# Kernel tuning notes

Hardware: AMD Instinct MI355X
Metric: run time of the kernel (lower is better)

Reference implementation:

```python
import jax, jax.numpy as jnp
import numpy as np

N_EMBD = 1024
N_HEAD = 16
HEAD_DIM = N_EMBD // N_HEAD  # 64
KV_RANK = 256
Q_RANK = 512
ROPE_DIM = 32
B, T = 2, 2048
EPS = 1e-6


def _rope_tables(T, dim):
    inv_freq = 1.0 / (10000.0 ** (np.arange(0, dim, 2, dtype=np.float32) / dim))
    t = np.arange(T, dtype=np.float32)
    freqs = np.outer(t, inv_freq)            # [T, dim/2]
    emb = np.concatenate([freqs, freqs], -1)  # [T, dim]
    return jnp.asarray(np.cos(emb)), jnp.asarray(np.sin(emb))


def _apply_rope(x, cos, sin):
    # x: [B, H, T, D]; cos/sin: [T, D]
    d2 = x.shape[-1] // 2
    x1, x2 = x[..., :d2], x[..., d2:]
    rot = jnp.concatenate([-x2, x1], axis=-1)
    return x * cos[None, None, :, :] + rot * sin[None, None, :, :]


def setup_inputs() -> dict:
    key = jax.random.key(0)
    ks = jax.random.split(key, 10)
    def w(k, fan_in, fan_out):
        return jax.random.normal(k, (fan_in, fan_out), dtype=jnp.float32) * (fan_in ** -0.5)
    return {
        "x": jax.random.normal(ks[0], (B, T, N_EMBD), dtype=jnp.float32),
        "W_kv": w(ks[1], N_EMBD, KV_RANK),
        "g_kv": jnp.ones((KV_RANK,), dtype=jnp.float32),
        "W_kdec": w(ks[2], KV_RANK, N_HEAD * HEAD_DIM),
        "W_vdec": w(ks[3], KV_RANK, N_HEAD * HEAD_DIM),
        "W_q": w(ks[4], N_EMBD, Q_RANK),
        "W_qdec": w(ks[5], Q_RANK, N_HEAD * HEAD_DIM),
        "W_krope": w(ks[6], N_EMBD, N_HEAD * ROPE_DIM),
        "W_qrope": w(ks[7], Q_RANK, N_HEAD * ROPE_DIM),
        "W_o": w(ks[8], N_HEAD * HEAD_DIM, N_EMBD),
    }


def reference(x, W_kv, g_kv, W_kdec, W_vdec, W_q, W_qdec, W_krope, W_qrope, W_o):
    Bx, Tx, C = x.shape
    # low-rank compression
    kv_c = x @ W_kv                                    # [B,T,R_kv]
    kv_c = kv_c * jax.lax.rsqrt(jnp.mean(kv_c * kv_c, axis=-1, keepdims=True) + EPS) * g_kv
    q_c = x @ W_q                                       # [B,T,R_q]
    # decompress to per-head content / rope parts -> [B,H,T,D]
    def heads(y, d):
        return y.reshape(Bx, Tx, N_HEAD, d).transpose(0, 2, 1, 3)
    k_content = heads(kv_c @ W_kdec, HEAD_DIM)
    v = heads(kv_c @ W_vdec, HEAD_DIM)
    q_content = heads(q_c @ W_qdec, HEAD_DIM)
    k_rope = heads(x @ W_krope, ROPE_DIM)
    q_rope = heads(q_c @ W_qrope, ROPE_DIM)
    cos, sin = _rope_tables(Tx, ROPE_DIM)
    q_rope = _apply_rope(q_rope, cos, sin)
    k_rope = _apply_rope(k_rope, cos, sin)
    q = jnp.concatenate([q_content, q_rope], axis=-1)   # [B,H,T,D+Dr]
    k = jnp.concatenate([k_content, k_rope], axis=-1)
    scale = 1.0 / jnp.sqrt(jnp.float32(q.shape[-1]))
    scores = jnp.einsum('bhqd,bhkd->bhqk', q, k) * scale  # [B,H,T,T]
    causal = jnp.tril(jnp.ones((Tx, Tx), dtype=bool))
    scores = jnp.where(causal[None, None], scores, jnp.float32(-jnp.inf))
    attn = jax.nn.softmax(scores, axis=-1)
    out = jnp.einsum('bhqk,bhkd->bhqd', attn, v)          # [B,H,T,D]
    out = out.transpose(0, 2, 1, 3).reshape(Bx, Tx, N_HEAD * HEAD_DIM)
    return out @ W_o
```

## Files before the change

### kernel.cpp

```cpp
#include <hip/hip_runtime.h>
#include <hip/hip_bf16.h>
#include <math.h>

#define Bz 2
#define Tz 2048
#define Cz 1024
#define Hz 16
#define Dz 64
#define Rz 32
#define KVR 256
#define QR 512
#define DQK 96
#define Mz (Bz*Tz)
#define BHT (Bz*Hz*Tz)
#define QK_SCALE 0.10206207261596577f
#define QK_SCALE2 0.14724538519399733f
#define THR2 11.541560327111707f

typedef __attribute__((ext_vector_type(8))) short short8;
typedef __attribute__((ext_vector_type(4))) float f32x4;
typedef __attribute__((ext_vector_type(4))) unsigned short ushort4v;

__device__ __forceinline__ unsigned short f2bf(float f) {
    union { float f; unsigned u; } un; un.f = f;
    unsigned r = un.u + 0x7FFF + ((un.u >> 16) & 1);
    return (unsigned short)(r >> 16);
}
__device__ __forceinline__ float bf2f(unsigned short h) {
    union { unsigned u; float f; } un; un.u = ((unsigned)h) << 16; return un.f;
}

__device__ __forceinline__ void gload_lds16(const void* g, void* l) {
    __builtin_amdgcn_global_load_lds(
        (const __attribute__((address_space(1))) unsigned int*)g,
        (__attribute__((address_space(3))) unsigned int*)l, 16, 0, 0);
}

__global__ __launch_bounds__(256) void conv_f32_bf16(const float* __restrict__ in,
                                                     unsigned short* __restrict__ out,
                                                     int n)
{
    int i = (blockIdx.x * 256 + threadIdx.x) * 4;
    if (i >= n) return;
    float4 v = *(const float4*)&in[i];
    ushort4v o = { f2bf(v.x), f2bf(v.y), f2bf(v.z), f2bf(v.w) };
    *(ushort4v*)&out[i] = o;
}

struct TDesc8 {
    const float* src[8];
    unsigned short* dst[8];
    int K[8], N[8];
    int tile0[9];
};

__global__ __launch_bounds__(256) void transpose_all(TDesc8 p)
{
    __shared__ float ts[32][33];
    int t = blockIdx.x;
    int wi = 0;
    #pragma unroll
    for (int i = 0; i < 7; i++) if (t >= p.tile0[i + 1]) wi = i + 1;
    int lt = t - p.tile0[wi];
    int K = p.K[wi], N = p.N[wi];
    int kT = K >> 5;
    int k0 = (lt % kT) * 32, n0 = (lt / kT) * 32;
    const float* in = p.src[wi];
    unsigned short* out = p.dst[wi];

    int tid = threadIdx.x;
    int r = tid >> 5, cc = tid & 31;
    #pragma unroll
    for (int l = 0; l < 4; l++)
        ts[r + l * 8][cc] = in[(size_t)(k0 + r + l * 8) * N + n0 + cc];
    __syncthreads();
    #pragma unroll
    for (int l = 0; l < 4; l++)
        out[(size_t)(n0 + r + l * 8) * K + k0 + cc] = f2bf(ts[cc][r + l * 8]);
}

template<int EMODE>
__global__ __launch_bounds__(64) void gemm1w(
    const unsigned short* __restrict__ A, const unsigned short* __restrict__ Wt,
    void* __restrict__ O0, void* __restrict__ O1, void* __restrict__ O2,
    int K, float scale)
{
    __shared__ __attribute__((aligned(16))) unsigned short As[64 * 64];
    __shared__ __attribute__((aligned(16))) unsigned short Bs[64 * 64];

    const int lane = threadIdx.x;
    const int c = lane & 15, g = lane >> 4;
    const int m0 = blockIdx.x * 64, n0 = blockIdx.y * 64;
    const int rl = lane >> 3, c8 = lane & 7;

    f32x4 acc[4][4] = {};

    auto stage = [&](int k0) {
        if (EMODE == 4) {
            int h = k0 >> 6;
            #pragma unroll
            for (int i = 0; i < 8; i++) {
                int m = m0 + i * 8 + rl;
                int b = m >> 11, t = m & (Tz - 1);
                gload_lds16(&A[(((size_t)b * Hz + h) * Tz + t) * 64 + c8 * 8],
                            &As[(i * 64 + lane) * 8]);
            }
        } else {
            #pragma unroll
            for (int i = 0; i < 8; i++)
                gload_lds16(&A[(size_t)(m0 + i * 8 + rl) * K + k0 + c8 * 8],
                            &As[(i * 64 + lane) * 8]);
        }
        #pragma unroll
        for (int i = 0; i < 8; i++)
            gload_lds16(&Wt[(size_t)(n0 + i * 8 + rl) * K + k0 + c8 * 8],
                        &Bs[(i * 64 + lane) * 8]);
    };

    stage(0);

    for (int k0 = 0; k0 < K; k0 += 64) {
        asm volatile("s_waitcnt vmcnt(0)" ::: "memory");
        __builtin_amdgcn_sched_barrier(0);

        short8 af[2][4], bfr[2][4];
        #pragma unroll
        for (int ks = 0; ks < 2; ks++) {
            #pragma unroll
            for (int mq = 0; mq < 4; mq++)
                af[ks][mq] = *(const short8*)&As[(mq * 16 + c) * 64 + ks * 32 + g * 8];
            #pragma unroll
            for (int nt = 0; nt < 4; nt++)
                bfr[ks][nt] = *(const short8*)&Bs[(nt * 16 + c) * 64 + ks * 32 + g * 8];
        }
        asm volatile("s_waitcnt lgkmcnt(0)" ::: "memory");
        __builtin_amdgcn_sched_barrier(0);

        if (k0 + 64 < K) stage(k0 + 64);

        __builtin_amdgcn_s_setprio(1);
        #pragma unroll
        for (int ks = 0; ks < 2; ks++)
            #pragma unroll
            for (int mq = 0; mq < 4; mq++)
                #pragma unroll
                for (int nt = 0; nt < 4; nt++)
                    acc[mq][nt] = __builtin_amdgcn_mfma_f32_16x16x32_bf16(
                        af[ks][mq], bfr[ks][nt], acc[mq][nt], 0, 0, 0);
        __builtin_amdgcn_s_setprio(0);
    }

    #pragma unroll
    for (int mq = 0; mq < 4; mq++) {
        #pragma unroll
        for (int r = 0; r < 4; r++) {
            int m = m0 + mq * 16 + g * 4 + r;
            int b = m >> 11, t = m & (Tz - 1);

            if (EMODE == 1) {
                if (n0 < 256) {
                    #pragma unroll
                    for (int nt = 0; nt < 4; nt++)
                        ((float*)O0)[(size_t)m * 256 + n0 + nt * 16 + c] = acc[mq][nt][r];
                } else if (n0 < 768) {
                    #pragma unroll
                    for (int nt = 0; nt < 4; nt++)
                        ((unsigned short*)O1)[(size_t)m * 512 + (n0 - 256) + nt * 16 + c] =
                            f2bf(acc[mq][nt][r]);
                } else {
                    float inv = __expf(-(float)c * 0.5756462732485114f);
                    float ang = (float)t * inv;
                    float cs = cosf(ang), sn = sinf(ang);
                    #pragma unroll
                    for (int np = 0; np < 4; np += 2) {
                        float v0 = acc[mq][np][r];
                        float v1 = acc[mq][np + 1][r];
                        int col0 = (n0 - 768) + np * 16;
                        int h = col0 >> 5;
                        size_t base = (((size_t)b * Hz + h) * Tz + t) * DQK + 64;
                        ((unsigned short*)O2)[base + c]      = f2bf(v0 * cs - v1 * sn);
                        ((unsigned short*)O2)[base + c + 16] = f2bf(v1 * cs + v0 * sn);
                    }
                }
            } else {
                #pragma unroll
                for (int nt = 0; nt < 4; nt++)
                    ((float*)O0)[(size_t)m * 1024 + n0 + nt * 16 + c] = acc[mq][nt][r];
            }
        }
    }
}

__global__ __launch_bounds__(64) void gemm1w23(
    const unsigned short* __restrict__ A2, const unsigned short* __restrict__ W2,
    unsigned short* __restrict__ qbb,
    const unsigned short* __restrict__ A3, const unsigned short* __restrict__ W3,
    unsigned short* __restrict__ kbb, unsigned short* __restrict__ vtb)
{
    const bool is2 = blockIdx.y < 24;
    const unsigned short* A  = is2 ? A2 : A3;
    const unsigned short* Wt = is2 ? W2 : W3;
    const int K = is2 ? QR : KVR;
    const int n0 = (is2 ? blockIdx.y : (blockIdx.y - 24)) * 64;

    __shared__ __attribute__((aligned(16))) unsigned short As[64 * 64];
    __shared__ __attribute__((aligned(16))) unsigned short Bs[64 * 64];

    const int lane = threadIdx.x;
    const int c = lane & 15, g = lane >> 4;
    const int m0 = blockIdx.x * 64;
    const int rl = lane >> 3, c8 = lane & 7;

    f32x4 acc[4][4] = {};

    auto stage = [&](int k0) {
        #pragma unroll
        for (int i = 0; i < 8; i++)
            gload_lds16(&A[(size_t)(m0 + i * 8 + rl) * K + k0 + c8 * 8],
                        &As[(i * 64 + lane) * 8]);
        #pragma unroll
        for (int i = 0; i < 8; i++)
            gload_lds16(&Wt[(size_t)(n0 + i * 8 + rl) * K + k0 + c8 * 8],
                        &Bs[(i * 64 + lane) * 8]);
    };

    stage(0);

    for (int k0 = 0; k0 < K; k0 += 64) {
        asm volatile("s_waitcnt vmcnt(0)" ::: "memory");
        __builtin_amdgcn_sched_barrier(0);

        short8 af[2][4], bfr[2][4];
        #pragma unroll
        for (int ks = 0; ks < 2; ks++) {
            #pragma unroll
            for (int mq = 0; mq < 4; mq++)
                af[ks][mq] = *(const short8*)&As[(mq * 16 + c) * 64 + ks * 32 + g * 8];
            #pragma unroll
            for (int nt = 0; nt < 4; nt++)
                bfr[ks][nt] = *(const short8*)&Bs[(nt * 16 + c) * 64 + ks * 32 + g * 8];
        }
        asm volatile("s_waitcnt lgkmcnt(0)" ::: "memory");
        __builtin_amdgcn_sched_barrier(0);

        if (k0 + 64 < K) stage(k0 + 64);

        __builtin_amdgcn_s_setprio(1);
        #pragma unroll
        for (int ks = 0; ks < 2; ks++)
            #pragma unroll
            for (int mq = 0; mq < 4; mq++)
                #pragma unroll
                for (int nt = 0; nt < 4; nt++)
                    acc[mq][nt] = __builtin_amdgcn_mfma_f32_16x16x32_bf16(
                        af[ks][mq], bfr[ks][nt], acc[mq][nt], 0, 0, 0);
        __builtin_amdgcn_s_setprio(0);
    }

    #pragma unroll
    for (int mq = 0; mq < 4; mq++) {
        #pragma unroll
        for (int r = 0; r < 4; r++) {
            int m = m0 + mq * 16 + g * 4 + r;
            int b = m >> 11, t = m & (Tz - 1);
            if (is2) {
                if (n0 < 1024) {
                    #pragma unroll
                    for (int nt = 0; nt < 4; nt++) {
                        int n = n0 + nt * 16 + c;
                        int h = n >> 6, dd = n & 63;
                        ((unsigned short*)qbb)[(((size_t)b * Hz + h) * Tz + t) * DQK + dd] =
                            f2bf(acc[mq][nt][r] * QK_SCALE2);
                    }
                } else {
                    float inv = __expf(-(float)c * 0.5756462732485114f);
                    float ang = (float)t * inv;
                    float cs = cosf(ang), sn = sinf(ang);
                    #pragma unroll
                    for (int np = 0; np < 4; np += 2) {
                        float v0 = acc[mq][np][r] * QK_SCALE2;
                        float v1 = acc[mq][np + 1][r] * QK_SCALE2;
                        int col0 = (n0 - 1024) + np * 16;
                        int h = col0 >> 5;
                        size_t base = (((size_t)b * Hz + h) * Tz + t) * DQK + 64;
                        qbb[base + c]      = f2bf(v0 * cs - v1 * sn);
                        qbb[base + c + 16] = f2bf(v1 * cs + v0 * sn);
                    }
                }
            } else {
                if (n0 < 1024) {
                    #pragma unroll
                    for (int nt = 0; nt < 4; nt++) {
                        int n = n0 + nt * 16 + c;
                        int h = n >> 6, dd = n & 63;
                        kbb[(((size_t)b * Hz + h) * Tz + t) * DQK + dd] = f2bf(acc[mq][nt][r]);
                    }
                } else {
                    #pragma unroll
                    for (int nt = 0; nt < 4; nt++) {
                        int n = (n0 - 1024) + nt * 16 + c;
                        int h = n >> 6, dd = n & 63;
                        vtb[(((size_t)b * Hz + h) * 64 + dd) * Tz + t] = f2bf(acc[mq][nt][r]);
                    }
                }
            }
        }
    }
}

__global__ __launch_bounds__(256) void rmsnorm_k(const float* __restrict__ kv,
                                                 const float* __restrict__ g,
                                                 unsigned short* __restrict__ outb)
{
    int row = blockIdx.x * 4 + (threadIdx.x >> 6);
    int lane = threadIdx.x & 63;
    const float* p = kv + (size_t)row * 256;
    float v[4];
    float ss = 0.f;
    #pragma unroll
    for (int i = 0; i < 4; i++) { v[i] = p[lane + i * 64]; ss += v[i] * v[i]; }
    #pragma unroll
    for (int o = 32; o > 0; o >>= 1) ss += __shfl_xor(ss, o);
    float r = rsqrtf(ss * (1.f / 256.f) + 1e-6f);
    #pragma unroll
    for (int i = 0; i < 4; i++)
        outb[(size_t)row * 256 + lane + i * 64] = f2bf(v[i] * r * g[lane + i * 64]);
}

#define PSTR 72

__global__ __launch_bounds__(256, 3) void attn_mfma(
    const unsigned short* __restrict__ q,
    const unsigned short* __restrict__ k,
    const unsigned short* __restrict__ vt,
    unsigned short* __restrict__ opart,
    float2* __restrict__ ml)
{
    __shared__ __attribute__((aligned(16))) unsigned short Ks[64 * 96];
    __shared__ __attribute__((aligned(16))) unsigned short Ps[4][16 * PSTR];

    int tid = threadIdx.x;
    int lane = tid & 63;
    int w = tid >> 6;
    int c = lane & 15, g = lane >> 4;

    int blk = blockIdx.x;
    int half = blk & 1;
    int s = blk >> 1;
    int bh = s & 31;
    int j = s >> 5;
    int qt = (j < 16) ? (31 - j) : (j - 16);
    int q0 = qt * 64;
    int ntiles = qt + 1;
    int nlo = ntiles >> 1;
    int tstart = half ? nlo : 0;
    int tend   = half ? ntiles : nlo;

    const unsigned short* qb = q + (size_t)bh * Tz * DQK;
    const unsigned short* kb = k + (size_t)bh * Tz * DQK;
    const unsigned short* vb = vt + (size_t)bh * 64 * Tz;
    unsigned short* ps = &Ps[w][0];

    int soff[3], sidx[3];
    #pragma unroll
    for (int i = 0; i < 3; i++) {
        int id2 = tid + i * 256;
        int srow = id2 / 12, sc8 = id2 % 12;
        soff[i] = srow * DQK + sc8 * 8;
        sidx[i] = (srow * 96 + sc8 * 8) ^ ((srow & 7) << 3);
    }

    short8 qf[3];
    {
        const unsigned short* qrow = qb + (size_t)(q0 + w * 16 + c) * DQK;
        #pragma unroll
        for (int kc = 0; kc < 3; kc++)
            qf[kc] = *(const short8*)(qrow + kc * 32 + g * 8);
    }

    short8 kreg[3];
    {
        size_t kix0 = (size_t)tstart * (64 * DQK);
        #pragma unroll
        for (int i = 0; i < 3; i++)
            kreg[i] = *(const short8*)&kb[kix0 + soff[i]];
        #pragma unroll
        for (int i = 0; i < 3; i++)
            *(short8*)&Ks[sidx[i]] = kreg[i];
    }
    __syncthreads();

    f32x4 oacc[4] = {};
    float mrun = -1e30f, lrun = 0.f;

    size_t kpre = (size_t)(tstart + 1) * (64 * DQK);
    size_t vix  = (size_t)c * Tz + g * 8 + (size_t)tstart * 64;

    for (int t = tstart; t < tend; t++) {
        bool more = (t + 1) < tend;

        if (more) {
            #pragma unroll
            for (int i = 0; i < 3; i++)
                kreg[i] = *(const short8*)&kb[kpre + soff[i]];
        }
        kpre += 64 * DQK;

        short8 vf[2][4];
        #pragma unroll
        for (int kc2 = 0; kc2 < 2; kc2++)
            #pragma unroll
            for (int nt = 0; nt < 4; nt++)
                vf[kc2][nt] = *(const short8*)&vb[vix + (size_t)nt * (16 * Tz) + kc2 * 32];
        vix += 64;

        f32x4 sacc[4] = {};
        __builtin_amdgcn_s_setprio(1);
        #pragma unroll
        for (int kc = 0; kc < 3; kc++) {
            #pragma unroll
            for (int nt = 0; nt < 4; nt++) {
                short8 kf = *(const short8*)&Ks[((nt * 16 + c) * 96 + kc * 32 + g * 8) ^ ((c & 7) << 3)];
                sacc[nt] = __builtin_amdgcn_mfma_f32_16x16x32_bf16(kf, qf[kc], sacc[nt], 0, 0, 0);
            }
        }
        __builtin_amdgcn_s_setprio(0);

        __syncthreads();
        if (more) {
            #pragma unroll
            for (int i = 0; i < 3; i++)
                *(short8*)&Ks[sidx[i]] = kreg[i];
        }

        if (t == ntiles - 1 && half) {
            #pragma unroll
            for (int nt = 0; nt < 4; nt++)
                #pragma unroll
                for (int r = 0; r < 4; r++)
                    if (nt * 16 + g * 4 + r > w * 16 + c)
                        sacc[nt][r] = -1e30f;
        }

        float pm = sacc[0][0];
        #pragma unroll
        for (int nt = 0; nt < 4; nt++)
            #pragma unroll
            for (int r = 0; r < 4; r++)
                pm = fmaxf(pm, sacc[nt][r]);
        pm = fmaxf(pm, __shfl_xor(pm, 16));
        pm = fmaxf(pm, __shfl_xor(pm, 32));

        bool need = pm > mrun + THR2;
        if (__ballot(need)) {
            float mn = fmaxf(mrun, pm);
            float sc = exp2f(mrun - mn);
            mrun = mn;
            float rs = 0.f;
            #pragma unroll
            for (int nt = 0; nt < 4; nt++)
                #pragma unroll
                for (int r = 0; r < 4; r++) {
                    sacc[nt][r] = exp2f(sacc[nt][r] - mrun);
                    rs += sacc[nt][r];
                }
            rs += __shfl_xor(rs, 16);
            rs += __shfl_xor(rs, 32);
            lrun = lrun * sc + rs;
            float scr[4];
            #pragma unroll
            for (int r = 0; r < 4; r++) scr[r] = __shfl(sc, g * 4 + r);
            #pragma unroll
            for (int nt = 0; nt < 4; nt++)
                #pragma unroll
                for (int r = 0; r < 4; r++)
                    oacc[nt][r] *= scr[r];
        } else {
            float rs = 0.f;
            #pragma unroll
            for (int nt = 0; nt < 4; nt++)
                #pragma unroll
                for (int r = 0; r < 4; r++) {
                    sacc[nt][r] = exp2f(sacc[nt][r] - mrun);
                    rs += sacc[nt][r];
                }
            rs += __shfl_xor(rs, 16);
            rs += __shfl_xor(rs, 32);
            lrun += rs;
        }

        #pragma unroll
        for (int nt = 0; nt < 4; nt++)
            #pragma unroll
            for (int rp = 0; rp < 2; rp++) {
                unsigned w32;
                asm("v_cvt_pk_bf16_f32 %0, %1, %2"
                    : "=v"(w32) : "v"(sacc[nt][2 * rp]), "v"(sacc[nt][2 * rp + 1]));
                *(unsigned*)&ps[c * PSTR + nt * 16 + g * 4 + 2 * rp] = w32;
            }
        __builtin_amdgcn_wave_barrier();

        __builtin_amdgcn_s_setprio(1);
        #pragma unroll
        for (int kc2 = 0; kc2 < 2; kc2++) {
            short8 pf = *(const short8*)&ps[c * PSTR + kc2 * 32 + g * 8];
            #pragma unroll
            for (int nt = 0; nt < 4; nt++)
                oacc[nt] = __builtin_amdgcn_mfma_f32_16x16x32_bf16(pf, vf[kc2][nt], oacc[nt], 0, 0, 0);
        }
        __builtin_amdgcn_s_setprio(0);
        __builtin_amdgcn_wave_barrier();

        __syncthreads();
    }

    size_t rowbase = (size_t)bh * Tz + q0 + w * 16;
    if (g == 0)
        ml[(size_t)half * BHT + rowbase + c] = make_float2(mrun, lrun);
    #pragma unroll
    for (int nt = 0; nt < 4; nt++)
        #pragma unroll
        for (int r = 0; r < 4; r++)
            opart[((size_t)half * BHT + rowbase + g * 4 + r) * 64 + nt * 16 + c] =
                f2bf(oacc[nt][r]);
}

__global__ __launch_bounds__(256) void attn_merge(
    const unsigned short* __restrict__ opart, const float2* __restrict__ ml,
    unsigned short* __restrict__ ob)
{
    size_t idx = (size_t)blockIdx.x * 256 + threadIdx.x;
    size_t row = idx >> 6;
    float2 a = ml[row], b = ml[BHT + row];
    float m = fmaxf(a.x, b.x);
    float s0 = exp2f(a.x - m), s1 = exp2f(b.x - m);
    float l = a.y * s0 + b.y * s1;
    float o0 = bf2f(opart[idx]), o1 = bf2f(opart[(size_t)BHT * 64 + idx]);
    ob[idx] = f2bf((o0 * s0 + o1 * s1) / l);
}

extern "C" void kernel_launch(void* const* d_in, const int* in_sizes, int n_in,
                              void* d_out, int out_size, void* d_ws, size_t ws_size,
                              hipStream_t stream)
{
    const float* x       = (const float*)d_in[0];
    const float* W_kv    = (const float*)d_in[1];
    const float* g_kv    = (const float*)d_in[2];
    const float* W_kdec  = (const float*)d_in[3];
    const float* W_vdec  = (const float*)d_in[4];
    const float* W_q     = (const float*)d_in[5];
    const float* W_qdec  = (const float*)d_in[6];
    const float* W_krope = (const float*)d_in[7];
    const float* W_qrope = (const float*)d_in[8];
    const float* W_o     = (const float*)d_in[9];
    float* out = (float*)d_out;

    float* kv_f32 = (float*)d_ws;
    unsigned short* us = (unsigned short*)(kv_f32 + (size_t)Mz * KVR);
    unsigned short* x_bf  = us;               us += (size_t)Mz * Cz;
    unsigned short* kv_bf = us;               us += (size_t)Mz * KVR;
    unsigned short* qc_bf = us;               us += (size_t)Mz * QR;
    unsigned short* qbb   = us;               us += (size_t)BHT * DQK;
    unsigned short* kbb   = us;               us += (size_t)BHT * DQK;
    unsigned short* vtb   = us;               us += (size_t)BHT * 64;
    unsigned short* ob    = us;               us += (size_t)BHT * 64;
    unsigned short* wc1 = us;                 us += (size_t)1280 * Cz;
    unsigned short* wc2 = us;                 us += (size_t)1536 * QR;
    unsigned short* wc3 = us;                 us += (size_t)2048 * KVR;
    unsigned short* woT = us;                 us += (size_t)Cz * Cz;
    unsigned short* opart = us;               us += (size_t)2 * BHT * 64;
    float2* mlbuf = (float2*)us;              us += (size_t)2 * BHT * 2;

    dim3 blk(256);

    conv_f32_bf16<<<dim3((Mz*Cz)/1024), blk, 0, stream>>>(x, x_bf, Mz*Cz);

    TDesc8 td;
    const float* tsrc[8] = {W_kv, W_q, W_krope, W_qdec, W_qrope, W_kdec, W_vdec, W_o};
    unsigned short* tdst[8] = {
        wc1, wc1 + (size_t)256 * Cz, wc1 + (size_t)768 * Cz,
        wc2, wc2 + (size_t)1024 * QR,
        wc3, wc3 + (size_t)1024 * KVR,
        woT };
    int tK[8] = {Cz, Cz, Cz, QR, QR, KVR, KVR, Cz};
    int tN[8] = {KVR, QR, Hz*Rz, Hz*Dz, Hz*Rz, Hz*Dz, Hz*Dz, Cz};
    int cum = 0;
    td.tile0[0] = 0;
    for (int i = 0; i < 8; i++) {
        td.src[i] = tsrc[i]; td.dst[i] = tdst[i]; td.K[i] = tK[i]; td.N[i] = tN[i];
        cum += (tK[i] / 32) * (tN[i] / 32);
        td.tile0[i + 1] = cum;
    }
    transpose_all<<<dim3(cum), blk, 0, stream>>>(td);

    gemm1w<1><<<dim3(Mz/64, 1280/64), dim3(64), 0, stream>>>(
        x_bf, wc1, kv_f32, qc_bf, kbb, Cz, 1.f);
    rmsnorm_k<<<dim3(Mz/4), blk, 0, stream>>>(kv_f32, g_kv, kv_bf);
    gemm1w23<<<dim3(Mz/64, 56), dim3(64), 0, stream>>>(
        qc_bf, wc2, qbb, kv_bf, wc3, kbb, vtb);
    attn_mfma<<<dim3(2048), blk, 0, stream>>>(qbb, kbb, vtb, opart, mlbuf);
    attn_merge<<<dim3((BHT * 64) / 256), blk, 0, stream>>>(opart, mlbuf, ob);
    gemm1w<4><<<dim3(Mz/64, Cz/64), dim3(64), 0, stream>>>(
        ob, woT, out, nullptr, nullptr, Cz, 1.f);
}
```

Before: 177.0 us.

## Drop split-KV attention and merge kernel; double-buffer K with overlapped QK and softmax

The attention kernel stops splitting each query tile's KV range across two blocks. It no longer writes partial outputs plus max/sum pairs for a separate merge kernel, and instead normalizes by the running sum and writes the final output directly. The K tile is double-buffered in LDS (KsA/KsB) so the QK MFMAs for the next tile are issued before softmax and PV of the current tile, overlapping matrix and vector work. This removes the merge launch and the partial-output traffic, but halves the grid to 1024 blocks and lowers the occupancy target to 2 blocks per CU, which may leave work unevenly spread across CUs.

```diff
diff --git a/kernel.cpp b/kernel.cpp
--- a/kernel.cpp
+++ b/kernel.cpp
@@ -329,14 +329,14 @@
 
 #define PSTR 72
 
-__global__ __launch_bounds__(256, 3) void attn_mfma(
+__global__ __launch_bounds__(256, 2) void attn_mfma(
     const unsigned short* __restrict__ q,
     const unsigned short* __restrict__ k,
     const unsigned short* __restrict__ vt,
-    unsigned short* __restrict__ opart,
-    float2* __restrict__ ml)
+    unsigned short* __restrict__ o)
 {
-    __shared__ __attribute__((aligned(16))) unsigned short Ks[64 * 96];
+    __shared__ __attribute__((aligned(16))) unsigned short KsA[64 * 96];
+    __shared__ __attribute__((aligned(16))) unsigned short KsB[64 * 96];
     __shared__ __attribute__((aligned(16))) unsigned short Ps[4][16 * PSTR];
 
     int tid = threadIdx.x;
@@ -344,17 +344,12 @@
     int w = tid >> 6;
     int c = lane & 15, g = lane >> 4;
 
-    int blk = blockIdx.x;
-    int half = blk & 1;
-    int s = blk >> 1;
+    int s = blockIdx.x;
     int bh = s & 31;
     int j = s >> 5;
     int qt = (j < 16) ? (31 - j) : (j - 16);
     int q0 = qt * 64;
     int ntiles = qt + 1;
-    int nlo = ntiles >> 1;
-    int tstart = half ? nlo : 0;
-    int tend   = half ? ntiles : nlo;
 
     const unsigned short* qb = q + (size_t)bh * Tz * DQK;
     const unsigned short* kb = k + (size_t)bh * Tz * DQK;
@@ -378,43 +373,11 @@
             qf[kc] = *(const short8*)(qrow + kc * 32 + g * 8);
     }
 
-    short8 kreg[3];
-    {
-        size_t kix0 = (size_t)tstart * (64 * DQK);
-        #pragma unroll
-        for (int i = 0; i < 3; i++)
-            kreg[i] = *(const short8*)&kb[kix0 + soff[i]];
-        #pragma unroll
-        for (int i = 0; i < 3; i++)
-            *(short8*)&Ks[sidx[i]] = kreg[i];
-    }
-    __syncthreads();
-
     f32x4 oacc[4] = {};
     float mrun = -1e30f, lrun = 0.f;
-
-    size_t kpre = (size_t)(tstart + 1) * (64 * DQK);
-    size_t vix  = (size_t)c * Tz + g * 8 + (size_t)tstart * 64;
-
-    for (int t = tstart; t < tend; t++) {
-        bool more = (t + 1) < tend;
-
-        if (more) {
-            #pragma unroll
-            for (int i = 0; i < 3; i++)
-                kreg[i] = *(const short8*)&kb[kpre + soff[i]];
-        }
-        kpre += 64 * DQK;
-
-        short8 vf[2][4];
-        #pragma unroll
-        for (int kc2 = 0; kc2 < 2; kc2++)
-            #pragma unroll
-            for (int nt = 0; nt < 4; nt++)
-                vf[kc2][nt] = *(const short8*)&vb[vix + (size_t)nt * (16 * Tz) + kc2 * 32];
-        vix += 64;
-
-        f32x4 sacc[4] = {};
+    f32x4 saccA[4] = {}, saccB[4] = {};
+
+    auto qk = [&](f32x4 (&sacc)[4], const unsigned short* Ks) {
         __builtin_amdgcn_s_setprio(1);
         #pragma unroll
         for (int kc = 0; kc < 3; kc++) {
@@ -425,15 +388,10 @@
             }
         }
         __builtin_amdgcn_s_setprio(0);
-
-        __syncthreads();
-        if (more) {
-            #pragma unroll
-            for (int i = 0; i < 3; i++)
-                *(short8*)&Ks[sidx[i]] = kreg[i];
-        }
-
-        if (t == ntiles - 1 && half) {
+    };
+
+    auto softmax_pv = [&](f32x4 (&sacc)[4], short8 (&vf)[2][4], bool diag) {
+        if (diag) {
             #pragma unroll
             for (int nt = 0; nt < 4; nt++)
                 #pragma unroll
@@ -441,7 +399,6 @@
                     if (nt * 16 + g * 4 + r > w * 16 + c)
                         sacc[nt][r] = -1e30f;
         }
-
         float pm = sacc[0][0];
         #pragma unroll
         for (int nt = 0; nt < 4; nt++)
@@ -510,33 +467,95 @@
         }
         __builtin_amdgcn_s_setprio(0);
         __builtin_amdgcn_wave_barrier();
-
+    };
+
+    short8 kreg[3];
+    #pragma unroll
+    for (int i = 0; i < 3; i++)
+        kreg[i] = *(const short8*)&kb[soff[i]];
+    #pragma unroll
+    for (int i = 0; i < 3; i++)
+        *(short8*)&KsA[sidx[i]] = kreg[i];
+    if (ntiles > 1) {
+        #pragma unroll
+        for (int i = 0; i < 3; i++)
+            kreg[i] = *(const short8*)&kb[(size_t)(64 * DQK) + soff[i]];
+    }
+    __syncthreads();
+    qk(saccA, KsA);
+
+    size_t kpre = (size_t)2 * (64 * DQK);
+    size_t vix  = (size_t)c * Tz + g * 8;
+
+    for (int t = 0; t < ntiles; t += 2) {
+        bool hasN1 = (t + 1) < ntiles;
+        bool hasN2 = (t + 2) < ntiles;
+        bool hasN3 = (t + 3) < ntiles;
+
+        if (hasN1) {
+            #pragma unroll
+            for (int i = 0; i < 3; i++)
+                *(short8*)&KsB[sidx[i]] = kreg[i];
+        }
+        if (hasN2) {
+            #pragma unroll
+            for (int i = 0; i < 3; i++)
+                kreg[i] = *(const short8*)&kb[kpre + soff[i]];
+        }
+        kpre += 64 * DQK;
         __syncthreads();
-    }
-
-    size_t rowbase = (size_t)bh * Tz + q0 + w * 16;
-    if (g == 0)
-        ml[(size_t)half * BHT + rowbase + c] = make_float2(mrun, lrun);
+
+        short8 vfA[2][4];
+        #pragma unroll
+        for (int kc2 = 0; kc2 < 2; kc2++)
+            #pragma unroll
+            for (int nt = 0; nt < 4; nt++)
+                vfA[kc2][nt] = *(const short8*)&vb[vix + (size_t)nt * (16 * Tz) + kc2 * 32];
+        vix += 64;
+
+        if (hasN1) qk(saccB, KsB);
+        softmax_pv(saccA, vfA, t == qt);
+        #pragma unroll
+        for (int nt = 0; nt < 4; nt++) saccA[nt] = f32x4{0.f, 0.f, 0.f, 0.f};
+
+        if (hasN1) {
+            if (hasN2) {
+                #pragma unroll
+                for (int i = 0; i < 3; i++)
+                    *(short8*)&KsA[sidx[i]] = kreg[i];
+            }
+            if (hasN3) {
+                #pragma unroll
+                for (int i = 0; i < 3; i++)
+                    kreg[i] = *(const short8*)&kb[kpre + soff[i]];
+            }
+            kpre += 64 * DQK;
+            __syncthreads();
+
+            short8 vfB[2][4];
+            #pragma unroll
+            for (int kc2 = 0; kc2 < 2; kc2++)
+                #pragma unroll
+                for (int nt = 0; nt < 4; nt++)
+                    vfB[kc2][nt] = *(const short8*)&vb[vix + (size_t)nt * (16 * Tz) + kc2 * 32];
+            vix += 64;
+
+            if (hasN2) qk(saccA, KsA);
+            softmax_pv(saccB, vfB, (t + 1) == qt);
+            #pragma unroll
+            for (int nt = 0; nt < 4; nt++) saccB[nt] = f32x4{0.f, 0.f, 0.f, 0.f};
+        }
+    }
+
+    float lr[4];
+    #pragma unroll
+    for (int r = 0; r < 4; r++) lr[r] = __shfl(lrun, g * 4 + r);
     #pragma unroll
     for (int nt = 0; nt < 4; nt++)
         #pragma unroll
         for (int r = 0; r < 4; r++)
-            opart[((size_t)half * BHT + rowbase + g * 4 + r) * 64 + nt * 16 + c] =
-                f2bf(oacc[nt][r]);
-}
-
-__global__ __launch_bounds__(256) void attn_merge(
-    const unsigned short* __restrict__ opart, const float2* __restrict__ ml,
-    unsigned short* __restrict__ ob)
-{
-    size_t idx = (size_t)blockIdx.x * 256 + threadIdx.x;
-    size_t row = idx >> 6;
-    float2 a = ml[row], b = ml[BHT + row];
-    float m = fmaxf(a.x, b.x);
-    float s0 = exp2f(a.x - m), s1 = exp2f(b.x - m);
-    float l = a.y * s0 + b.y * s1;
-    float o0 = bf2f(opart[idx]), o1 = bf2f(opart[(size_t)BHT * 64 + idx]);
-    ob[idx] = f2bf((o0 * s0 + o1 * s1) / l);
+            o[((size_t)bh * Tz + q0 + w * 16 + g * 4 + r) * 64 + nt * 16 + c] =
+                f2bf(oacc[nt][r] / lr[r]);
 }
 
 extern "C" void kernel_launch(void* const* d_in, const int* in_sizes, int n_in,
@@ -568,8 +587,6 @@
     unsigned short* wc2 = us;                 us += (size_t)1536 * QR;
     unsigned short* wc3 = us;                 us += (size_t)2048 * KVR;
     unsigned short* woT = us;                 us += (size_t)Cz * Cz;
-    unsigned short* opart = us;               us += (size_t)2 * BHT * 64;
-    float2* mlbuf = (float2*)us;              us += (size_t)2 * BHT * 2;
 
     dim3 blk(256);
 
@@ -598,8 +615,7 @@
     rmsnorm_k<<<dim3(Mz/4), blk, 0, stream>>>(kv_f32, g_kv, kv_bf);
     gemm1w23<<<dim3(Mz/64, 56), dim3(64), 0, stream>>>(
         qc_bf, wc2, qbb, kv_bf, wc3, kbb, vtb);
-    attn_mfma<<<dim3(2048), blk, 0, stream>>>(qbb, kbb, vtb, opart, mlbuf);
-    attn_merge<<<dim3((BHT * 64) / 256), blk, 0, stream>>>(opart, mlbuf, ob);
+    attn_mfma<<<dim3(1024), blk, 0, stream>>>(qbb, kbb, vtb, ob);
     gemm1w<4><<<dim3(Mz/64, Cz/64), dim3(64), 0, stream>>>(
         ob, woT, out, nullptr, nullptr, Cz, 1.f);
 }
```

After: 166.9 us. 1.06x faster.

## Drop split-KV attention halves and merge kernel, double-buffer K tile in LDS

Applied to the files above, without the earlier changes.

Each attention block now handles a full causal KV range for its query tile rather than half of it. This removes the partial-output and max/sum buffers and the separate merge kernel, and the output is normalised directly in the epilogue. The K tile in LDS becomes double-buffered, so each iteration needs one barrier instead of two. The cost is half as many blocks (1024) with longer per-block work, which lowers parallelism and load balance on a large GPU.

```diff
diff --git a/kernel.cpp b/kernel.cpp
--- a/kernel.cpp
+++ b/kernel.cpp
@@ -13,7 +13,6 @@
 #define DQK 96
 #define Mz (Bz*Tz)
 #define BHT (Bz*Hz*Tz)
-#define QK_SCALE 0.10206207261596577f
 #define QK_SCALE2 0.14724538519399733f
 #define THR2 11.541560327111707f
 
@@ -25,9 +24,6 @@
     union { float f; unsigned u; } un; un.f = f;
     unsigned r = un.u + 0x7FFF + ((un.u >> 16) & 1);
     return (unsigned short)(r >> 16);
-}
-__device__ __forceinline__ float bf2f(unsigned short h) {
-    union { unsigned u; float f; } un; un.u = ((unsigned)h) << 16; return un.f;
 }
 
 __device__ __forceinline__ void gload_lds16(const void* g, void* l) {
@@ -333,10 +329,9 @@
     const unsigned short* __restrict__ q,
     const unsigned short* __restrict__ k,
     const unsigned short* __restrict__ vt,
-    unsigned short* __restrict__ opart,
-    float2* __restrict__ ml)
-{
-    __shared__ __attribute__((aligned(16))) unsigned short Ks[64 * 96];
+    unsigned short* __restrict__ o)
+{
+    __shared__ __attribute__((aligned(16))) unsigned short Ks[2][64 * 96];
     __shared__ __attribute__((aligned(16))) unsigned short Ps[4][16 * PSTR];
 
     int tid = threadIdx.x;
@@ -344,17 +339,12 @@
     int w = tid >> 6;
     int c = lane & 15, g = lane >> 4;
 
-    int blk = blockIdx.x;
-    int half = blk & 1;
-    int s = blk >> 1;
+    int s = blockIdx.x;
     int bh = s & 31;
     int j = s >> 5;
     int qt = (j < 16) ? (31 - j) : (j - 16);
     int q0 = qt * 64;
     int ntiles = qt + 1;
-    int nlo = ntiles >> 1;
-    int tstart = half ? nlo : 0;
-    int tend   = half ? ntiles : nlo;
 
     const unsigned short* qb = q + (size_t)bh * Tz * DQK;
     const unsigned short* kb = k + (size_t)bh * Tz * DQK;
@@ -379,40 +369,33 @@
     }
 
     short8 kreg[3];
-    {
-        size_t kix0 = (size_t)tstart * (64 * DQK);
-        #pragma unroll
-        for (int i = 0; i < 3; i++)
-            kreg[i] = *(const short8*)&kb[kix0 + soff[i]];
-        #pragma unroll
-        for (int i = 0; i < 3; i++)
-            *(short8*)&Ks[sidx[i]] = kreg[i];
-    }
+    #pragma unroll
+    for (int i = 0; i < 3; i++)
+        kreg[i] = *(const short8*)&kb[soff[i]];
+    #pragma unroll
+    for (int i = 0; i < 3; i++)
+        *(short8*)&Ks[0][sidx[i]] = kreg[i];
     __syncthreads();
 
     f32x4 oacc[4] = {};
     float mrun = -1e30f, lrun = 0.f;
 
-    size_t kpre = (size_t)(tstart + 1) * (64 * DQK);
-    size_t vix  = (size_t)c * Tz + g * 8 + (size_t)tstart * 64;
-
-    for (int t = tstart; t < tend; t++) {
-        bool more = (t + 1) < tend;
+    for (int t = 0; t < ntiles; t++) {
+        int cur = t & 1;
+        int kt0 = t * 64;
+        bool more = (t + 1) < ntiles;
 
         if (more) {
             #pragma unroll
             for (int i = 0; i < 3; i++)
-                kreg[i] = *(const short8*)&kb[kpre + soff[i]];
-        }
-        kpre += 64 * DQK;
-
+                kreg[i] = *(const short8*)&kb[(size_t)(kt0 + 64) * DQK + soff[i]];
+        }
         short8 vf[2][4];
         #pragma unroll
         for (int kc2 = 0; kc2 < 2; kc2++)
             #pragma unroll
             for (int nt = 0; nt < 4; nt++)
-                vf[kc2][nt] = *(const short8*)&vb[vix + (size_t)nt * (16 * Tz) + kc2 * 32];
-        vix += 64;
+                vf[kc2][nt] = *(const short8*)&vb[(size_t)(nt * 16 + c) * Tz + kt0 + kc2 * 32 + g * 8];
 
         f32x4 sacc[4] = {};
         __builtin_amdgcn_s_setprio(1);
@@ -420,20 +403,13 @@
         for (int kc = 0; kc < 3; kc++) {
             #pragma unroll
             for (int nt = 0; nt < 4; nt++) {
-                short8 kf = *(const short8*)&Ks[((nt * 16 + c) * 96 + kc * 32 + g * 8) ^ ((c & 7) << 3)];
+                short8 kf = *(const short8*)&Ks[cur][((nt * 16 + c) * 96 + kc * 32 + g * 8) ^ ((c & 7) << 3)];
                 sacc[nt] = __builtin_amdgcn_mfma_f32_16x16x32_bf16(kf, qf[kc], sacc[nt], 0, 0, 0);
             }
         }
         __builtin_amdgcn_s_setprio(0);
 
-        __syncthreads();
-        if (more) {
-            #pragma unroll
-            for (int i = 0; i < 3; i++)
-                *(short8*)&Ks[sidx[i]] = kreg[i];
-        }
-
-        if (t == ntiles - 1 && half) {
+        if (kt0 == q0) {
             #pragma unroll
             for (int nt = 0; nt < 4; nt++)
                 #pragma unroll
@@ -511,32 +487,23 @@
         __builtin_amdgcn_s_setprio(0);
         __builtin_amdgcn_wave_barrier();
 
-        __syncthreads();
-    }
-
-    size_t rowbase = (size_t)bh * Tz + q0 + w * 16;
-    if (g == 0)
-        ml[(size_t)half * BHT + rowbase + c] = make_float2(mrun, lrun);
+        if (more) {
+            #pragma unroll
+            for (int i = 0; i < 3; i++)
+                *(short8*)&Ks[1 - cur][sidx[i]] = kreg[i];
+            __syncthreads();
+        }
+    }
+
+    float lr[4];
+    #pragma unroll
+    for (int r = 0; r < 4; r++) lr[r] = __shfl(lrun, g * 4 + r);
     #pragma unroll
     for (int nt = 0; nt < 4; nt++)
         #pragma unroll
         for (int r = 0; r < 4; r++)
-            opart[((size_t)half * BHT + rowbase + g * 4 + r) * 64 + nt * 16 + c] =
-                f2bf(oacc[nt][r]);
-}
-
-__global__ __launch_bounds__(256) void attn_merge(
-    const unsigned short* __restrict__ opart, const float2* __restrict__ ml,
-    unsigned short* __restrict__ ob)
-{
-    size_t idx = (size_t)blockIdx.x * 256 + threadIdx.x;
-    size_t row = idx >> 6;
-    float2 a = ml[row], b = ml[BHT + row];
-    float m = fmaxf(a.x, b.x);
-    float s0 = exp2f(a.x - m), s1 = exp2f(b.x - m);
-    float l = a.y * s0 + b.y * s1;
-    float o0 = bf2f(opart[idx]), o1 = bf2f(opart[(size_t)BHT * 64 + idx]);
-    ob[idx] = f2bf((o0 * s0 + o1 * s1) / l);
+            o[((size_t)bh * Tz + q0 + w * 16 + g * 4 + r) * 64 + nt * 16 + c] =
+                f2bf(oacc[nt][r] / lr[r]);
 }
 
 extern "C" void kernel_launch(void* const* d_in, const int* in_sizes, int n_in,
@@ -568,8 +535,6 @@
     unsigned short* wc2 = us;                 us += (size_t)1536 * QR;
     unsigned short* wc3 = us;                 us += (size_t)2048 * KVR;
     unsigned short* woT = us;                 us += (size_t)Cz * Cz;
-    unsigned short* opart = us;               us += (size_t)2 * BHT * 64;
-    float2* mlbuf = (float2*)us;              us += (size_t)2 * BHT * 2;
 
     dim3 blk(256);
 
@@ -598,8 +563,7 @@
     rmsnorm_k<<<dim3(Mz/4), blk, 0, stream>>>(kv_f32, g_kv, kv_bf);
     gemm1w23<<<dim3(Mz/64, 56), dim3(64), 0, stream>>>(
         qc_bf, wc2, qbb, kv_bf, wc3, kbb, vtb);
-    attn_mfma<<<dim3(2048), blk, 0, stream>>>(qbb, kbb, vtb, opart, mlbuf);
-    attn_merge<<<dim3((BHT * 64) / 256), blk, 0, stream>>>(opart, mlbuf, ob);
+    attn_mfma<<<dim3(1024), blk, 0, stream>>>(qbb, kbb, vtb, ob);
     gemm1w<4><<<dim3(Mz/64, Cz/64), dim3(64), 0, stream>>>(
         ob, woT, out, nullptr, nullptr, Cz, 1.f);
 }
```

After: 163.5 us, median of 2. 7.6% less time.
